# Kernel tuning notes

Measured on AMD Instinct MI355X. Metric: run time of the kernel, lower is better.

The kernel has to match this reference:

```python
import jax, jax.numpy as jnp
import numpy as np

B, T, DM, DK = 16, 2048, 1024, 128

def setup_inputs() -> dict:
    key = jax.random.key(0)
    k1, k2, k3, k4 = jax.random.split(key, 4)
    x = jax.random.normal(k1, (B, T, DM), dtype=jnp.float32)
    # Linear(dm, dk, bias=False) weights, stored as [dm, dk] for x @ W
    scale = 1.0 / np.sqrt(DM)
    W_q = jax.random.normal(k2, (DM, DK), dtype=jnp.float32) * scale
    W_k = jax.random.normal(k3, (DM, DK), dtype=jnp.float32) * scale
    W_v = jax.random.normal(k4, (DM, DK), dtype=jnp.float32) * scale
    return {"x": x, "W_q": W_q, "W_k": W_k, "W_v": W_v}

def reference(x, W_q, W_k, W_v):
    # q, k, v: [B, T, DK]
    q = jnp.einsum('btd,dk->btk', x, W_q)
    k = jnp.einsum('btd,dk->btk', x, W_k)
    v = jnp.einsum('btd,dk->btk', x, W_v)
    dk = k.shape[-1]
    # scores: [B, T, T], scaled by dk**-0.5
    wei = jnp.einsum('bqk,bsk->bqs', q, k) * (dk ** -0.5)
    # causal mask (tril == 0 -> -inf)
    causal = jnp.tril(jnp.ones((q.shape[1], q.shape[1]), dtype=bool))
    wei = jnp.where(causal, wei, -jnp.inf)
    wei = jax.nn.softmax(wei, axis=-1)
    out = jnp.einsum('bqs,bsk->bqk', wei, v)  # [B, T, DK]
    return out
```

## Files before the change

kernel.cpp:

```cpp
#include <hip/hip_runtime.h>
#include <hip/hip_bf16.h>

#define NB 16
#define NT 2048
#define NDM 1024
#define NDK 128

typedef __bf16 bf16;
typedef bf16 bf16x4 __attribute__((ext_vector_type(4)));
typedef bf16 bf16x8 __attribute__((ext_vector_type(8)));
typedef float f32x4 __attribute__((ext_vector_type(4)));

__device__ inline bf16 to_bf16(float f) {
    __hip_bfloat16 h = __float2bfloat16(f);
    return *reinterpret_cast<bf16*>(&h);
}

__global__ __launch_bounds__(256) void transpose_w_kernel(
        const float* __restrict__ Wq, const float* __restrict__ Wk,
        const float* __restrict__ Wv, bf16* __restrict__ Wt) {
    int idx = blockIdx.x * 256 + threadIdx.x;
    int w = idx >> 17;
    int r = idx & (NDM * NDK - 1);
    int k = r >> 7;
    int n = r & (NDK - 1);
    const float* W = (w == 0) ? Wq : ((w == 1) ? Wk : Wv);
    Wt[(size_t)w * NDK * NDM + (size_t)n * NDM + k] = to_bf16(W[(size_t)k * NDK + n]);
}

__global__ __launch_bounds__(256) void proj_kernel(
        const float* __restrict__ x, const bf16* __restrict__ Wt,
        bf16* __restrict__ qkv) {
    __shared__ bf16 As[128][40];
    __shared__ bf16 Bs[128][40];
    const int tid = threadIdx.x;
    const int lane = tid & 63;
    const int wave = tid >> 6;
    const int wr = wave >> 1, wc = wave & 1;
    const int r16 = lane & 15, kg = lane >> 4;
    const int mb = blockIdx.x;
    const int w = blockIdx.y;
    const float* xA = x + (size_t)mb * 128 * NDM;
    const bf16* Bt = Wt + (size_t)w * NDK * NDM;

    f32x4 acc[4][4];
#pragma unroll
    for (int m = 0; m < 4; m++)
#pragma unroll
        for (int n = 0; n < 4; n++) acc[m][n] = (f32x4){0.f, 0.f, 0.f, 0.f};

    for (int k0 = 0; k0 < NDM; k0 += 32) {
#pragma unroll
        for (int p = 0; p < 4; p++) {
            int row = p * 32 + (tid >> 3);
            int c4 = (tid & 7) * 4;
            const float4 v = *reinterpret_cast<const float4*>(&xA[(size_t)row * NDM + k0 + c4]);
            bf16x4 bv = { to_bf16(v.x), to_bf16(v.y), to_bf16(v.z), to_bf16(v.w) };
            *reinterpret_cast<bf16x4*>(&As[row][c4]) = bv;
        }
#pragma unroll
        for (int p = 0; p < 2; p++) {
            int idx = (p * 256 + tid) * 8;
            int n = idx >> 5;
            int kk = idx & 31;
            *reinterpret_cast<bf16x8*>(&Bs[n][kk]) =
                *reinterpret_cast<const bf16x8*>(&Bt[(size_t)n * NDM + k0 + kk]);
        }
        __syncthreads();
        bf16x8 af[4], bfr[4];
#pragma unroll
        for (int m = 0; m < 4; m++)
            af[m] = *reinterpret_cast<const bf16x8*>(&As[wr * 64 + m * 16 + r16][kg * 8]);
#pragma unroll
        for (int n = 0; n < 4; n++)
            bfr[n] = *reinterpret_cast<const bf16x8*>(&Bs[wc * 64 + n * 16 + r16][kg * 8]);
#pragma unroll
        for (int m = 0; m < 4; m++)
#pragma unroll
            for (int n = 0; n < 4; n++)
                acc[m][n] = __builtin_amdgcn_mfma_f32_16x16x32_bf16(af[m], bfr[n], acc[m][n], 0, 0, 0);
        __syncthreads();
    }

    bf16* outw = qkv + (size_t)w * (size_t)(NB * NT) * NDK;
#pragma unroll
    for (int m = 0; m < 4; m++) {
        int rowb = mb * 128 + wr * 64 + m * 16 + kg * 4;
#pragma unroll
        for (int n = 0; n < 4; n++) {
            int col = wc * 64 + n * 16 + r16;
#pragma unroll
            for (int r = 0; r < 4; r++)
                outw[(size_t)(rowb + r) * NDK + col] = to_bf16(acc[m][n][r]);
        }
    }
}

__global__ __launch_bounds__(256) void transpose_v_kernel(
        const bf16* __restrict__ V, bf16* __restrict__ Vt) {
    __shared__ bf16 Tl[64][136];
    const int tid = threadIdx.x;
    const int tb = blockIdx.x, b = blockIdx.y;
    const int t0 = tb * 64;
    const size_t ibase = (size_t)b * NT * NDK;
    const size_t obase = (size_t)b * NDK * NT;
#pragma unroll
    for (int p = 0; p < 4; p++) {
        int idx = p * 256 + tid;
        int row = idx >> 4, c = idx & 15;
        *reinterpret_cast<bf16x8*>(&Tl[row][c * 8]) =
            *reinterpret_cast<const bf16x8*>(&V[ibase + (size_t)(t0 + row) * NDK + c * 8]);
    }
    __syncthreads();
#pragma unroll
    for (int p = 0; p < 4; p++) {
        int idx = p * 256 + tid;
        int d = idx >> 3, c = idx & 7;
        bf16x8 v;
#pragma unroll
        for (int j = 0; j < 8; j++) v[j] = Tl[c * 8 + j][d];
        *reinterpret_cast<bf16x8*>(&Vt[obase + (size_t)d * NT + t0 + c * 8]) = v;
    }
}

__global__ __launch_bounds__(256) void attn_kernel(
        const bf16* __restrict__ Q, const bf16* __restrict__ K,
        const bf16* __restrict__ Vt, float* __restrict__ out) {
    __shared__ bf16 Ks[64][128];
    __shared__ bf16 Vs[128][64];
    __shared__ bf16 Ps[4][16][72];
    const int tid = threadIdx.x, lane = tid & 63, wave = tid >> 6;
    const int r16 = lane & 15, kg = lane >> 4;

    const int bid = blockIdx.x;
    const int xcd = bid & 7;
    const int j = bid >> 3;
    const int b = xcd * 2 + (j & 1);
    const int qb = (NT / 64 - 1) - (j >> 1);
    const int q0 = qb * 64;
    const size_t baseB = (size_t)b * NT * NDK;
    const size_t baseVt = (size_t)b * NDK * NT;

    const float scale = 0.08838834764831843f;
    bf16x8 qf[4];
    const int qrow = q0 + wave * 16 + r16;
#pragma unroll
    for (int kc = 0; kc < 4; kc++) {
        bf16x8 raw = *reinterpret_cast<const bf16x8*>(&Q[baseB + (size_t)qrow * NDK + kc * 32 + kg * 8]);
#pragma unroll
        for (int jj = 0; jj < 8; jj++) raw[jj] = to_bf16((float)raw[jj] * scale);
        qf[kc] = raw;
    }

    f32x4 o[8];
#pragma unroll
    for (int n = 0; n < 8; n++) o[n] = (f32x4){0.f, 0.f, 0.f, 0.f};
    float mrow[4] = {-INFINITY, -INFINITY, -INFINITY, -INFINITY};
    float lrow[4] = {0.f, 0.f, 0.f, 0.f};

    int krow[4], kcol[4], vrow[4], vcol[4];
#pragma unroll
    for (int i = 0; i < 4; i++) {
        int idx = i * 256 + tid;
        krow[i] = idx >> 4; kcol[i] = idx & 15;
        vrow[i] = idx >> 3; vcol[i] = idx & 7;
    }

    const int nsteps = qb + 1;

    bf16x8 kreg[4], vreg[4];
#pragma unroll
    for (int i = 0; i < 4; i++) {
        kreg[i] = *reinterpret_cast<const bf16x8*>(&K[baseB + (size_t)krow[i] * NDK + kcol[i] * 8]);
        vreg[i] = *reinterpret_cast<const bf16x8*>(&Vt[baseVt + (size_t)vrow[i] * NT + vcol[i] * 8]);
    }

    for (int s = 0; s < nsteps; s++) {
        __syncthreads();
#pragma unroll
        for (int i = 0; i < 4; i++)
            *reinterpret_cast<bf16x8*>(&Ks[krow[i]][(kcol[i] ^ (krow[i] & 7)) * 8]) = kreg[i];
#pragma unroll
        for (int i = 0; i < 4; i++)
            *reinterpret_cast<bf16x8*>(&Vs[vrow[i]][(vcol[i] ^ (vrow[i] & 7)) * 8]) = vreg[i];
        __syncthreads();

        if (s + 1 < nsteps) {
            const int kv0n = (s + 1) * 64;
#pragma unroll
            for (int i = 0; i < 4; i++) {
                kreg[i] = *reinterpret_cast<const bf16x8*>(&K[baseB + (size_t)(kv0n + krow[i]) * NDK + kcol[i] * 8]);
                vreg[i] = *reinterpret_cast<const bf16x8*>(&Vt[baseVt + (size_t)vrow[i] * NT + kv0n + vcol[i] * 8]);
            }
        }

        const int kv0 = s * 64;
        f32x4 sfr[4];
#pragma unroll
        for (int n = 0; n < 4; n++) sfr[n] = (f32x4){0.f, 0.f, 0.f, 0.f};
#pragma unroll
        for (int n = 0; n < 4; n++) {
            const int krw = n * 16 + r16;
#pragma unroll
            for (int kc = 0; kc < 4; kc++) {
                bf16x8 kf = *reinterpret_cast<const bf16x8*>(&Ks[krw][((kc * 4 + kg) ^ (krw & 7)) * 8]);
                sfr[n] = __builtin_amdgcn_mfma_f32_16x16x32_bf16(qf[kc], kf, sfr[n], 0, 0, 0);
            }
        }

        if (s == nsteps - 1) {
#pragma unroll
            for (int n = 0; n < 4; n++) {
#pragma unroll
                for (int r = 0; r < 4; r++) {
                    int col = kv0 + n * 16 + r16;
                    int row = q0 + wave * 16 + kg * 4 + r;
                    if (col > row) sfr[n][r] = -INFINITY;
                }
            }
        }

        float pmax[4] = {-INFINITY, -INFINITY, -INFINITY, -INFINITY};
#pragma unroll
        for (int n = 0; n < 4; n++)
#pragma unroll
            for (int r = 0; r < 4; r++) pmax[r] = fmaxf(pmax[r], sfr[n][r]);
#pragma unroll
        for (int d = 1; d < 16; d <<= 1)
#pragma unroll
            for (int r = 0; r < 4; r++)
                pmax[r] = fmaxf(pmax[r], __shfl_xor(pmax[r], d, 64));

        float gmax = -INFINITY;
#pragma unroll
        for (int r = 0; r < 4; r++) gmax = fmaxf(gmax, pmax[r] - mrow[r]);
        if (__any(gmax > 0.f)) {
#pragma unroll
            for (int r = 0; r < 4; r++) {
                float mnew = fmaxf(mrow[r], pmax[r]);
                float corr = __expf(mrow[r] - mnew);
                mrow[r] = mnew;
                lrow[r] *= corr;
#pragma unroll
                for (int n = 0; n < 8; n++) o[n][r] *= corr;
            }
        }

        float psum[4] = {0.f, 0.f, 0.f, 0.f};
#pragma unroll
        for (int n = 0; n < 4; n++) {
#pragma unroll
            for (int r = 0; r < 4; r++) {
                float pv = __expf(sfr[n][r] - mrow[r]);
                psum[r] += pv;
                Ps[wave][kg * 4 + r][n * 16 + r16] = to_bf16(pv);
            }
        }
#pragma unroll
        for (int d = 1; d < 16; d <<= 1)
#pragma unroll
            for (int r = 0; r < 4; r++)
                psum[r] += __shfl_xor(psum[r], d, 64);
#pragma unroll
        for (int r = 0; r < 4; r++) lrow[r] += psum[r];

#pragma unroll
        for (int kc2 = 0; kc2 < 2; kc2++) {
            bf16x8 pf = *reinterpret_cast<const bf16x8*>(&Ps[wave][r16][kc2 * 32 + kg * 8]);
#pragma unroll
            for (int n = 0; n < 8; n++) {
                const int vrw = n * 16 + r16;
                bf16x8 vf = *reinterpret_cast<const bf16x8*>(&Vs[vrw][((kc2 * 4 + kg) ^ (vrw & 7)) * 8]);
                o[n] = __builtin_amdgcn_mfma_f32_16x16x32_bf16(pf, vf, o[n], 0, 0, 0);
            }
        }
    }

    float inv[4];
#pragma unroll
    for (int r = 0; r < 4; r++) inv[r] = 1.0f / lrow[r];
#pragma unroll
    for (int n = 0; n < 8; n++)
#pragma unroll
        for (int r = 0; r < 4; r++) {
            int row = q0 + wave * 16 + kg * 4 + r;
            int col = n * 16 + r16;
            out[baseB + (size_t)row * NDK + col] = o[n][r] * inv[r];
        }
}

extern "C" void kernel_launch(void* const* d_in, const int* in_sizes, int n_in,
                              void* d_out, int out_size, void* d_ws, size_t ws_size,
                              hipStream_t stream) {
    const float* x  = (const float*)d_in[0];
    const float* Wq = (const float*)d_in[1];
    const float* Wk = (const float*)d_in[2];
    const float* Wv = (const float*)d_in[3];
    float* out = (float*)d_out;

    char* ws = (char*)d_ws;
    bf16* Wt  = (bf16*)ws;
    bf16* qkv = (bf16*)(ws + (1ull << 20));
    bf16* Vtg = (bf16*)(ws + (26ull << 20));

    transpose_w_kernel<<<(3 * NDM * NDK) / 256, 256, 0, stream>>>(Wq, Wk, Wv, Wt);

    dim3 g1((NB * NT) / 128, 3);
    proj_kernel<<<g1, 256, 0, stream>>>(x, Wt, qkv);

    bf16* Qp = qkv;
    bf16* Kp = qkv + (size_t)(NB * NT) * NDK;
    bf16* Vp = qkv + 2 * (size_t)(NB * NT) * NDK;

    dim3 gt(NT / 64, NB);
    transpose_v_kernel<<<gt, 256, 0, stream>>>(Vp, Vtg);

    attn_kernel<<<dim3((NT / 64) * NB), 256, 0, stream>>>(Qp, Kp, Vtg, out);
}
```

Baseline: 121.0 us.

## Fuse V transpose into projection, double-buffer attention K/V tiles, transpose score MFMA

The projection kernel now writes V directly in transposed [b][d][t] layout, which removes the separate transpose_v kernel launch and its extra global round trip. The attention kernel double-buffers K/V tiles in shared memory, so each step needs one barrier and the next tile's LDS store overlaps compute. The score MFMA operands are swapped so that each lane holds one query row's scores. Row max and sum then need only two cross-lane shuffles instead of four per row, and P is written to LDS as packed vectors. Shared memory use doubles for K/V, which may reduce occupancy.

```diff
diff --git a/kernel.cpp b/kernel.cpp
--- a/kernel.cpp
+++ b/kernel.cpp
@@ -30,7 +30,7 @@
 
 __global__ __launch_bounds__(256) void proj_kernel(
         const float* __restrict__ x, const bf16* __restrict__ Wt,
-        bf16* __restrict__ qkv) {
+        bf16* __restrict__ qkv, bf16* __restrict__ Vt) {
     __shared__ bf16 As[128][40];
     __shared__ bf16 Bs[128][40];
     const int tid = threadIdx.x;
@@ -82,52 +82,42 @@
         __syncthreads();
     }
 
-    bf16* outw = qkv + (size_t)w * (size_t)(NB * NT) * NDK;
-#pragma unroll
-    for (int m = 0; m < 4; m++) {
-        int rowb = mb * 128 + wr * 64 + m * 16 + kg * 4;
-#pragma unroll
-        for (int n = 0; n < 4; n++) {
-            int col = wc * 64 + n * 16 + r16;
-#pragma unroll
-            for (int r = 0; r < 4; r++)
-                outw[(size_t)(rowb + r) * NDK + col] = to_bf16(acc[m][n][r]);
-        }
-    }
-}
-
-__global__ __launch_bounds__(256) void transpose_v_kernel(
-        const bf16* __restrict__ V, bf16* __restrict__ Vt) {
-    __shared__ bf16 Tl[64][136];
-    const int tid = threadIdx.x;
-    const int tb = blockIdx.x, b = blockIdx.y;
-    const int t0 = tb * 64;
-    const size_t ibase = (size_t)b * NT * NDK;
-    const size_t obase = (size_t)b * NDK * NT;
-#pragma unroll
-    for (int p = 0; p < 4; p++) {
-        int idx = p * 256 + tid;
-        int row = idx >> 4, c = idx & 15;
-        *reinterpret_cast<bf16x8*>(&Tl[row][c * 8]) =
-            *reinterpret_cast<const bf16x8*>(&V[ibase + (size_t)(t0 + row) * NDK + c * 8]);
-    }
-    __syncthreads();
-#pragma unroll
-    for (int p = 0; p < 4; p++) {
-        int idx = p * 256 + tid;
-        int d = idx >> 3, c = idx & 7;
-        bf16x8 v;
-#pragma unroll
-        for (int j = 0; j < 8; j++) v[j] = Tl[c * 8 + j][d];
-        *reinterpret_cast<bf16x8*>(&Vt[obase + (size_t)d * NT + t0 + c * 8]) = v;
+    if (w < 2) {
+        bf16* outw = qkv + (size_t)w * (size_t)(NB * NT) * NDK;
+#pragma unroll
+        for (int m = 0; m < 4; m++) {
+            int rowb = mb * 128 + wr * 64 + m * 16 + kg * 4;
+#pragma unroll
+            for (int n = 0; n < 4; n++) {
+                int col = wc * 64 + n * 16 + r16;
+#pragma unroll
+                for (int r = 0; r < 4; r++)
+                    outw[(size_t)(rowb + r) * NDK + col] = to_bf16(acc[m][n][r]);
+            }
+        }
+    } else {
+        const int b = mb >> 4;
+        const int tl0 = (mb & 15) * 128 + wr * 64;
+        bf16* Vb = Vt + (size_t)b * NDK * NT;
+#pragma unroll
+        for (int m = 0; m < 4; m++) {
+            int tl = tl0 + m * 16 + kg * 4;
+#pragma unroll
+            for (int n = 0; n < 4; n++) {
+                int d = wc * 64 + n * 16 + r16;
+                bf16x4 pv = { to_bf16(acc[m][n][0]), to_bf16(acc[m][n][1]),
+                              to_bf16(acc[m][n][2]), to_bf16(acc[m][n][3]) };
+                *reinterpret_cast<bf16x4*>(&Vb[(size_t)d * NT + tl]) = pv;
+            }
+        }
     }
 }
 
 __global__ __launch_bounds__(256) void attn_kernel(
         const bf16* __restrict__ Q, const bf16* __restrict__ K,
         const bf16* __restrict__ Vt, float* __restrict__ out) {
-    __shared__ bf16 Ks[64][128];
-    __shared__ bf16 Vs[128][64];
+    __shared__ bf16 Ks[2][64][128];
+    __shared__ bf16 Vs[2][128][64];
     __shared__ bf16 Ps[4][16][72];
     const int tid = threadIdx.x, lane = tid & 63, wave = tid >> 6;
     const int r16 = lane & 15, kg = lane >> 4;
@@ -143,10 +133,10 @@
 
     const float scale = 0.08838834764831843f;
     bf16x8 qf[4];
-    const int qrow = q0 + wave * 16 + r16;
+    const int qglob = q0 + wave * 16 + r16;
 #pragma unroll
     for (int kc = 0; kc < 4; kc++) {
-        bf16x8 raw = *reinterpret_cast<const bf16x8*>(&Q[baseB + (size_t)qrow * NDK + kc * 32 + kg * 8]);
+        bf16x8 raw = *reinterpret_cast<const bf16x8*>(&Q[baseB + (size_t)qglob * NDK + kc * 32 + kg * 8]);
 #pragma unroll
         for (int jj = 0; jj < 8; jj++) raw[jj] = to_bf16((float)raw[jj] * scale);
         qf[kc] = raw;
@@ -155,8 +145,8 @@
     f32x4 o[8];
 #pragma unroll
     for (int n = 0; n < 8; n++) o[n] = (f32x4){0.f, 0.f, 0.f, 0.f};
-    float mrow[4] = {-INFINITY, -INFINITY, -INFINITY, -INFINITY};
-    float lrow[4] = {0.f, 0.f, 0.f, 0.f};
+    float mrun = -INFINITY;
+    float lrun = 0.f;
 
     int krow[4], kcol[4], vrow[4], vcol[4];
 #pragma unroll
@@ -167,34 +157,30 @@
     }
 
     const int nsteps = qb + 1;
-
     bf16x8 kreg[4], vreg[4];
 #pragma unroll
     for (int i = 0; i < 4; i++) {
         kreg[i] = *reinterpret_cast<const bf16x8*>(&K[baseB + (size_t)krow[i] * NDK + kcol[i] * 8]);
         vreg[i] = *reinterpret_cast<const bf16x8*>(&Vt[baseVt + (size_t)vrow[i] * NT + vcol[i] * 8]);
     }
+#pragma unroll
+    for (int i = 0; i < 4; i++) {
+        *reinterpret_cast<bf16x8*>(&Ks[0][krow[i]][(kcol[i] ^ (krow[i] & 7)) * 8]) = kreg[i];
+        *reinterpret_cast<bf16x8*>(&Vs[0][vrow[i]][(vcol[i] ^ (vrow[i] & 7)) * 8]) = vreg[i];
+    }
+    if (nsteps > 1) {
+#pragma unroll
+        for (int i = 0; i < 4; i++) {
+            kreg[i] = *reinterpret_cast<const bf16x8*>(&K[baseB + (size_t)(64 + krow[i]) * NDK + kcol[i] * 8]);
+            vreg[i] = *reinterpret_cast<const bf16x8*>(&Vt[baseVt + (size_t)vrow[i] * NT + 64 + vcol[i] * 8]);
+        }
+    }
+    __syncthreads();
 
     for (int s = 0; s < nsteps; s++) {
-        __syncthreads();
-#pragma unroll
-        for (int i = 0; i < 4; i++)
-            *reinterpret_cast<bf16x8*>(&Ks[krow[i]][(kcol[i] ^ (krow[i] & 7)) * 8]) = kreg[i];
-#pragma unroll
-        for (int i = 0; i < 4; i++)
-            *reinterpret_cast<bf16x8*>(&Vs[vrow[i]][(vcol[i] ^ (vrow[i] & 7)) * 8]) = vreg[i];
-        __syncthreads();
-
-        if (s + 1 < nsteps) {
-            const int kv0n = (s + 1) * 64;
-#pragma unroll
-            for (int i = 0; i < 4; i++) {
-                kreg[i] = *reinterpret_cast<const bf16x8*>(&K[baseB + (size_t)(kv0n + krow[i]) * NDK + kcol[i] * 8]);
-                vreg[i] = *reinterpret_cast<const bf16x8*>(&Vt[baseVt + (size_t)vrow[i] * NT + kv0n + vcol[i] * 8]);
-            }
-        }
-
+        const int cur = s & 1;
         const int kv0 = s * 64;
+
         f32x4 sfr[4];
 #pragma unroll
         for (int n = 0; n < 4; n++) sfr[n] = (f32x4){0.f, 0.f, 0.f, 0.f};
@@ -203,66 +189,57 @@
             const int krw = n * 16 + r16;
 #pragma unroll
             for (int kc = 0; kc < 4; kc++) {
-                bf16x8 kf = *reinterpret_cast<const bf16x8*>(&Ks[krw][((kc * 4 + kg) ^ (krw & 7)) * 8]);
-                sfr[n] = __builtin_amdgcn_mfma_f32_16x16x32_bf16(qf[kc], kf, sfr[n], 0, 0, 0);
+                bf16x8 kf = *reinterpret_cast<const bf16x8*>(&Ks[cur][krw][((kc * 4 + kg) ^ (krw & 7)) * 8]);
+                sfr[n] = __builtin_amdgcn_mfma_f32_16x16x32_bf16(kf, qf[kc], sfr[n], 0, 0, 0);
             }
         }
 
         if (s == nsteps - 1) {
 #pragma unroll
-            for (int n = 0; n < 4; n++) {
-#pragma unroll
-                for (int r = 0; r < 4; r++) {
-                    int col = kv0 + n * 16 + r16;
-                    int row = q0 + wave * 16 + kg * 4 + r;
-                    if (col > row) sfr[n][r] = -INFINITY;
-                }
-            }
-        }
-
-        float pmax[4] = {-INFINITY, -INFINITY, -INFINITY, -INFINITY};
-#pragma unroll
-        for (int n = 0; n < 4; n++)
-#pragma unroll
-            for (int r = 0; r < 4; r++) pmax[r] = fmaxf(pmax[r], sfr[n][r]);
-#pragma unroll
-        for (int d = 1; d < 16; d <<= 1)
-#pragma unroll
-            for (int r = 0; r < 4; r++)
-                pmax[r] = fmaxf(pmax[r], __shfl_xor(pmax[r], d, 64));
-
-        float gmax = -INFINITY;
-#pragma unroll
-        for (int r = 0; r < 4; r++) gmax = fmaxf(gmax, pmax[r] - mrow[r]);
-        if (__any(gmax > 0.f)) {
+            for (int n = 0; n < 4; n++)
+#pragma unroll
+                for (int r = 0; r < 4; r++)
+                    if (kv0 + n * 16 + kg * 4 + r > qglob) sfr[n][r] = -INFINITY;
+        }
+
+        float pm = -INFINITY;
+#pragma unroll
+        for (int n = 0; n < 4; n++) {
+            float t0 = fmaxf(fmaxf(sfr[n][0], sfr[n][1]), fmaxf(sfr[n][2], sfr[n][3]));
+            pm = fmaxf(pm, t0);
+        }
+        pm = fmaxf(pm, __shfl_xor(pm, 16, 64));
+        pm = fmaxf(pm, __shfl_xor(pm, 32, 64));
+
+        if (__any(pm > mrun)) {
+            float mnew = fmaxf(mrun, pm);
+            float corr = __expf(mrun - mnew);
+            mrun = mnew;
+            lrun *= corr;
+            float co[4];
+#pragma unroll
+            for (int r = 0; r < 4; r++) co[r] = __shfl(corr, kg * 4 + r, 64);
+#pragma unroll
+            for (int n = 0; n < 8; n++)
+#pragma unroll
+                for (int r = 0; r < 4; r++) o[n][r] *= co[r];
+        }
+
+        float ps = 0.f;
+#pragma unroll
+        for (int n = 0; n < 4; n++) {
+            bf16x4 pw;
 #pragma unroll
             for (int r = 0; r < 4; r++) {
-                float mnew = fmaxf(mrow[r], pmax[r]);
-                float corr = __expf(mrow[r] - mnew);
-                mrow[r] = mnew;
-                lrow[r] *= corr;
-#pragma unroll
-                for (int n = 0; n < 8; n++) o[n][r] *= corr;
-            }
-        }
-
-        float psum[4] = {0.f, 0.f, 0.f, 0.f};
-#pragma unroll
-        for (int n = 0; n < 4; n++) {
-#pragma unroll
-            for (int r = 0; r < 4; r++) {
-                float pv = __expf(sfr[n][r] - mrow[r]);
-                psum[r] += pv;
-                Ps[wave][kg * 4 + r][n * 16 + r16] = to_bf16(pv);
-            }
-        }
-#pragma unroll
-        for (int d = 1; d < 16; d <<= 1)
-#pragma unroll
-            for (int r = 0; r < 4; r++)
-                psum[r] += __shfl_xor(psum[r], d, 64);
-#pragma unroll
-        for (int r = 0; r < 4; r++) lrow[r] += psum[r];
+                float pv = __expf(sfr[n][r] - mrun);
+                ps += pv;
+                pw[r] = to_bf16(pv);
+            }
+            *reinterpret_cast<bf16x4*>(&Ps[wave][r16][n * 16 + kg * 4]) = pw;
+        }
+        ps += __shfl_xor(ps, 16, 64);
+        ps += __shfl_xor(ps, 32, 64);
+        lrun += ps;
 
 #pragma unroll
         for (int kc2 = 0; kc2 < 2; kc2++) {
@@ -270,22 +247,40 @@
 #pragma unroll
             for (int n = 0; n < 8; n++) {
                 const int vrw = n * 16 + r16;
-                bf16x8 vf = *reinterpret_cast<const bf16x8*>(&Vs[vrw][((kc2 * 4 + kg) ^ (vrw & 7)) * 8]);
+                bf16x8 vf = *reinterpret_cast<const bf16x8*>(&Vs[cur][vrw][((kc2 * 4 + kg) ^ (vrw & 7)) * 8]);
                 o[n] = __builtin_amdgcn_mfma_f32_16x16x32_bf16(pf, vf, o[n], 0, 0, 0);
             }
         }
-    }
-
-    float inv[4];
-#pragma unroll
-    for (int r = 0; r < 4; r++) inv[r] = 1.0f / lrow[r];
+
+        if (s + 1 < nsteps) {
+#pragma unroll
+            for (int i = 0; i < 4; i++) {
+                *reinterpret_cast<bf16x8*>(&Ks[1 - cur][krow[i]][(kcol[i] ^ (krow[i] & 7)) * 8]) = kreg[i];
+                *reinterpret_cast<bf16x8*>(&Vs[1 - cur][vrow[i]][(vcol[i] ^ (vrow[i] & 7)) * 8]) = vreg[i];
+            }
+            if (s + 2 < nsteps) {
+                const int kv2 = (s + 2) * 64;
+#pragma unroll
+                for (int i = 0; i < 4; i++) {
+                    kreg[i] = *reinterpret_cast<const bf16x8*>(&K[baseB + (size_t)(kv2 + krow[i]) * NDK + kcol[i] * 8]);
+                    vreg[i] = *reinterpret_cast<const bf16x8*>(&Vt[baseVt + (size_t)vrow[i] * NT + kv2 + vcol[i] * 8]);
+                }
+            }
+        }
+        __syncthreads();
+    }
+
+    float linv = 1.0f / lrun;
+    float li[4];
+#pragma unroll
+    for (int r = 0; r < 4; r++) li[r] = __shfl(linv, kg * 4 + r, 64);
 #pragma unroll
     for (int n = 0; n < 8; n++)
 #pragma unroll
         for (int r = 0; r < 4; r++) {
             int row = q0 + wave * 16 + kg * 4 + r;
             int col = n * 16 + r16;
-            out[baseB + (size_t)row * NDK + col] = o[n][r] * inv[r];
+            out[baseB + (size_t)row * NDK + col] = o[n][r] * li[r];
         }
 }
 
@@ -306,14 +301,10 @@
     transpose_w_kernel<<<(3 * NDM * NDK) / 256, 256, 0, stream>>>(Wq, Wk, Wv, Wt);
 
     dim3 g1((NB * NT) / 128, 3);
-    proj_kernel<<<g1, 256, 0, stream>>>(x, Wt, qkv);
+    proj_kernel<<<g1, 256, 0, stream>>>(x, Wt, qkv, Vtg);
 
     bf16* Qp = qkv;
     bf16* Kp = qkv + (size_t)(NB * NT) * NDK;
-    bf16* Vp = qkv + 2 * (size_t)(NB * NT) * NDK;
-
-    dim3 gt(NT / 64, NB);
-    transpose_v_kernel<<<gt, 256, 0, stream>>>(Vp, Vtg);
 
     attn_kernel<<<dim3((NT / 64) * NB), 256, 0, stream>>>(Qp, Kp, Vtg, out);
 }
```

Result: faster. 102.9 us (-14.9%).
